# Optimization experiments

Hardware: AMD Instinct MI355X
Metric: run time of the kernel (lower is better)

The kernel has to match this reference:

```python
import jax, jax.numpy as jnp
import numpy as np

N = 50000      # nodes
E = 800000     # edges (before self-loops)
F_IN = 128     # args.nsegment
H = 4          # args.nhead
C = 32         # args.dhidden
OUT = 64       # output_dim
G = 64         # number of graphs in batch
NEG = 0.2      # args.negslope (and GATv2 internal leaky-relu slope, PyG default 0.2)


def setup_inputs() -> dict:
    key = jax.random.key(0)
    ks = jax.random.split(key, 8)
    def w(k, i, o):
        return jax.random.normal(k, (i, o), jnp.float32) / np.sqrt(i)
    x = jax.random.normal(ks[0], (N, F_IN), jnp.float32)
    edge_index = jax.random.randint(ks[1], (2, E), 0, N, dtype=jnp.int32)
    batch = jnp.sort(jax.random.randint(ks[2], (N,), 0, G, dtype=jnp.int32))
    d = dict(x=x, edge_index=edge_index, batch=batch)
    # layer dims: (in_dim, heads, out_per_head, concat)
    dims = [(F_IN, H, C, True), (H * C, H, C, True), (H * C, 1, OUT, False)]
    for li, (fi, h, c, concat) in enumerate(dims):
        k1, k2, k3 = jax.random.split(ks[3 + li], 3)
        d[f"Wl{li}"] = w(k1, fi, h * c)
        d[f"Wr{li}"] = w(k2, fi, h * c)
        d[f"att{li}"] = jax.random.normal(k3, (h, c), jnp.float32) / np.sqrt(c)
        d[f"b{li}"] = jnp.zeros((h * c if concat else c,), jnp.float32)
    return d


def _gat_layer(x, src, tgt, Wl, Wr, att, b, concat):
    """GATv2Conv: e_ij = att . leaky_relu(Wl x_j + Wr x_i); softmax over edges into i;
    out_i = sum_j alpha_ij * (Wl x_j). src/tgt include self-loops."""
    n = x.shape[0]
    h, c = att.shape
    xl = (x @ Wl).reshape(n, h, c)                 # source transform [N,h,c]
    xr = (x @ Wr).reshape(n, h, c)                 # target transform [N,h,c]
    g = jax.nn.leaky_relu(xl[src] + xr[tgt], NEG)  # [Etot,h,c]
    score = jnp.einsum('ehc,hc->eh', g, att)       # [Etot,h]
    smax = jax.ops.segment_max(score, tgt, num_segments=n)
    ex = jnp.exp(score - smax[tgt])
    den = jax.ops.segment_sum(ex, tgt, num_segments=n)
    alpha = ex / den[tgt]                          # per-target softmax [Etot,h]
    out = jax.ops.segment_sum(xl[src] * alpha[:, :, None], tgt, num_segments=n)
    out = out.reshape(n, h * c) if concat else out.mean(axis=1)
    return out + b


def _forward(x, edge_index, batch, params):
    n = x.shape[0]
    loops = jnp.arange(n, dtype=edge_index.dtype)  # PyG add_self_loops=True
    src = jnp.concatenate([edge_index[0], loops])
    tgt = jnp.concatenate([edge_index[1], loops])
    for Wl, Wr, att, b, concat in params:
        x = _gat_layer(x, src, tgt, Wl, Wr, att, b, concat)
        x = jax.nn.leaky_relu(x, NEG)  # dropout p is identity in eval mode
    ssum = jax.ops.segment_sum(x, batch, num_segments=G)
    cnt = jax.ops.segment_sum(jnp.ones((n,), x.dtype), batch, num_segments=G)
    return ssum / jnp.maximum(cnt, 1.0)[:, None]   # global_mean_pool -> [G, OUT]


def reference(x, edge_index, batch, Wl0, Wr0, att0, b0, Wl1, Wr1, att1, b1, Wl2, Wr2, att2, b2):
    params = [(Wl0, Wr0, att0, b0, True),
              (Wl1, Wr1, att1, b1, True),
              (Wl2, Wr2, att2, b2, False)]
    return _forward(x, edge_index, batch, params)
```

## Files before the change

kernel.cpp:

```cpp
#include <hip/hip_runtime.h>
#include <hip/hip_fp16.h>
#include <math.h>

#define NEGSLOPE 0.2f

__device__ __forceinline__ float lrelu(float x) { return x > 0.f ? x : NEGSLOPE * x; }

__global__ void k_count(const int* __restrict__ tgt, int* __restrict__ deg, int e) {
    int i = blockIdx.x * 256 + threadIdx.x;
    if (i < e) atomicAdd(&deg[tgt[i]], 1);
}
__global__ __launch_bounds__(256) void k_scanA(const int* __restrict__ deg, int* __restrict__ rowptr,
                                               int* __restrict__ bsums, int n) {
    __shared__ int s[256];
    int t = threadIdx.x;
    int base = blockIdx.x * 4096 + t * 16;
    int pre[16];
    int sum = 0;
    for (int i = 0; i < 16; ++i) {
        int idx = base + i;
        int v = (idx < n) ? (deg[idx] + 1) : 0;
        pre[i] = sum;
        sum += v;
    }
    s[t] = sum;
    __syncthreads();
    for (int off = 1; off < 256; off <<= 1) {
        int v = (t >= off) ? s[t - off] : 0;
        __syncthreads();
        s[t] += v;
        __syncthreads();
    }
    int tbase = s[t] - sum;
    for (int i = 0; i < 16; ++i) {
        int idx = base + i;
        if (idx < n) rowptr[idx] = tbase + pre[i];
    }
    if (t == 0) bsums[blockIdx.x] = s[255];
}
__global__ void k_scanB(int* __restrict__ bsums, int* __restrict__ rowptr, int nblk, int n) {
    if (threadIdx.x == 0 && blockIdx.x == 0) {
        int run = 0;
        for (int i = 0; i < nblk; ++i) { int v = bsums[i]; bsums[i] = run; run += v; }
        rowptr[n] = run;
    }
}
__global__ void k_scanC(int* __restrict__ rowptr, const int* __restrict__ bsums,
                        int* __restrict__ edst, int* __restrict__ cursor, int n) {
    int i = blockIdx.x * 256 + threadIdx.x;
    if (i < n) {
        int rp = rowptr[i] + bsums[i >> 12];
        rowptr[i] = rp;
        edst[rp] = i;
        cursor[i] = rp + 1;
    }
}
__global__ void k_scatter(const int* __restrict__ src, const int* __restrict__ tgt,
                          int* __restrict__ cursor, int* __restrict__ edst, int e) {
    int i = blockIdx.x * 256 + threadIdx.x;
    if (i < e) { int p = atomicAdd(&cursor[tgt[i]], 1); edst[p] = src[i]; }
}

template<int KOUT>
__global__ __launch_bounds__(256) void k_gemm_fused(const float* __restrict__ Ain,
        const float* __restrict__ W0, const float* __restrict__ W1,
        __half* __restrict__ out0, float* __restrict__ out1, int n) {
    __shared__ float Ast[32][132];
    __shared__ float Wt[32][132];
    int t = threadIdx.x;
    int ct = blockIdx.y;
    int w = t >> 6, lane = t & 63;
    int rg = (lane >> 3) + 8 * (w & 1);
    int cg = (lane & 7) + 8 * (w >> 1);
    int r0 = rg * 8, c0 = cg * 8;
    int row0 = blockIdx.x * 128;

    float acc[8][8] = {};
    for (int kc = 0; kc < 4; ++kc) {
        int kb = kc * 32;
        __syncthreads();
        for (int i = 0; i < 4; ++i) {
            int idx = t + 256 * i;
            int r = idx >> 3, kq = idx & 7;
            float4 v = make_float4(0.f, 0.f, 0.f, 0.f);
            int gr = row0 + r;
            if (gr < n) v = *(const float4*)(Ain + (size_t)gr * 128 + kb + 4 * kq);
            Ast[4 * kq + 0][r] = v.x; Ast[4 * kq + 1][r] = v.y;
            Ast[4 * kq + 2][r] = v.z; Ast[4 * kq + 3][r] = v.w;
        }
        for (int i = 0; i < 4; ++i) {
            int idx = t + 256 * i;
            int k = idx >> 5, cq = idx & 31;
            float4 v;
            if (KOUT == 128) {
                const float* W = ct ? W1 : W0;
                v = *(const float4*)(W + (size_t)(kb + k) * 128 + 4 * cq);
            } else {
                const float* W = (cq < 16) ? W0 : W1;
                int c = (cq < 16) ? 4 * cq : 4 * (cq - 16);
                v = *(const float4*)(W + (size_t)(kb + k) * 64 + c);
            }
            *(float4*)&Wt[k][4 * cq] = v;
        }
        __syncthreads();
#pragma unroll 2
        for (int k = 0; k < 32; ++k) {
            float a_[8], b_[8];
            *(float4*)&a_[0] = *(const float4*)&Ast[k][r0];
            *(float4*)&a_[4] = *(const float4*)&Ast[k][r0 + 4];
            *(float4*)&b_[0] = *(const float4*)&Wt[k][c0];
            *(float4*)&b_[4] = *(const float4*)&Wt[k][c0 + 4];
#pragma unroll
            for (int i = 0; i < 8; ++i)
#pragma unroll
                for (int j = 0; j < 8; ++j)
                    acc[i][j] += a_[i] * b_[j];
        }
    }
    bool asHalf = (KOUT == 128) ? (ct == 0) : (cg < 8);
    int c = (KOUT == 128) ? c0 : ((cg < 8) ? c0 : c0 - 64);
    for (int i = 0; i < 8; ++i) {
        int gr = row0 + r0 + i;
        if (gr >= n) break;
        if (asHalf) {
            union { uint4 u; __half2 h[4]; } pk;
#pragma unroll
            for (int j = 0; j < 4; ++j)
                pk.h[j] = __float22half2_rn(make_float2(acc[i][2 * j], acc[i][2 * j + 1]));
            *(uint4*)(out0 + (size_t)gr * KOUT + c) = pk.u;
        } else {
            *(float4*)(out1 + (size_t)gr * KOUT + c)     = *(float4*)&acc[i][0];
            *(float4*)(out1 + (size_t)gr * KOUT + c + 4) = *(float4*)&acc[i][4];
        }
    }
}

template<int H, int C>
__global__ __launch_bounds__(256) void k_agg(const __half* __restrict__ xl, const float* __restrict__ xr,
                                             const float* __restrict__ att, const float* __restrict__ bias,
                                             const int* __restrict__ rowptr, const int* __restrict__ edst,
                                             float* __restrict__ yout, int n) {
    constexpr int F = H * C;
    constexpr int VEC = F / 16;
    constexpr int L = C / VEC;
    int lane = threadIdx.x & 63;
    int wave = threadIdx.x >> 6;
    int s = lane & 15;
    int node = blockIdx.x * 16 + wave * 4 + (lane >> 4);
    bool valid = node < n;
    int nodeSafe = valid ? node : 0;
    int ch = s * VEC;

    float u[VEC], av[VEC], acc[VEC];
#pragma unroll
    for (int j = 0; j < VEC; ++j) {
        u[j] = xr[(size_t)nodeSafe * F + ch + j];
        av[j] = att[ch + j];
        acc[j] = 0.f;
    }
    int e0 = rowptr[nodeSafe];
    int deg = valid ? (rowptr[nodeSafe + 1] - e0) : 0;
    int maxdeg = deg;
    maxdeg = max(maxdeg, __shfl_xor(maxdeg, 16));
    maxdeg = max(maxdeg, __shfl_xor(maxdeg, 32));
    float ssum = 0.f;

    auto loadrow = [&](int src, float* v) {
        const __half* p = xl + (size_t)src * F + ch;
        if constexpr (VEC == 8) {
            union { uint4 u4; __half2 h[4]; } pk;
            pk.u4 = *(const uint4*)p;
#pragma unroll
            for (int j = 0; j < 4; ++j) {
                float2 f = __half22float2(pk.h[j]);
                v[2 * j] = f.x; v[2 * j + 1] = f.y;
            }
        } else {
            union { uint2 u2; __half2 h[2]; } pk;
            pk.u2 = *(const uint2*)p;
#pragma unroll
            for (int j = 0; j < 2; ++j) {
                float2 f = __half22float2(pk.h[j]);
                v[2 * j] = f.x; v[2 * j + 1] = f.y;
            }
        }
    };
    auto dot = [&](const float* v) {
        float p = 0.f;
#pragma unroll
        for (int j = 0; j < VEC; ++j) p += lrelu(v[j] + u[j]) * av[j];
        return p;
    };
    auto accum = [&](float w, const float* v) {
        ssum += w;
#pragma unroll
        for (int j = 0; j < VEC; ++j) acc[j] += w * v[j];
    };

    for (int base = 0; base < maxdeg; base += 16) {
        int cnt = deg - base;
        if (cnt > 16) cnt = 16;
        int idxreg = (s < cnt) ? edst[e0 + base + s] : nodeSafe;
        int mcnt = cnt;
        mcnt = max(mcnt, __shfl_xor(mcnt, 16));
        mcnt = max(mcnt, __shfl_xor(mcnt, 32));
        int gbase = lane & 48;
        int i = 0;
        for (; i + 4 <= mcnt; i += 4) {
            int s0 = __shfl(idxreg, gbase + i);
            int s1 = __shfl(idxreg, gbase + i + 1);
            int s2 = __shfl(idxreg, gbase + i + 2);
            int s3 = __shfl(idxreg, gbase + i + 3);
            float v0[VEC], v1[VEC], v2[VEC], v3[VEC];
            loadrow(s0, v0); loadrow(s1, v1); loadrow(s2, v2); loadrow(s3, v3);
            float p0 = dot(v0), p1 = dot(v1), p2 = dot(v2), p3 = dot(v3);
#pragma unroll
            for (int off = 1; off < L; off <<= 1) {
                p0 += __shfl_xor(p0, off);
                p1 += __shfl_xor(p1, off);
                p2 += __shfl_xor(p2, off);
                p3 += __shfl_xor(p3, off);
            }
            float w0 = (i + 0 < cnt) ? __expf(p0) : 0.f;
            float w1 = (i + 1 < cnt) ? __expf(p1) : 0.f;
            float w2 = (i + 2 < cnt) ? __expf(p2) : 0.f;
            float w3 = (i + 3 < cnt) ? __expf(p3) : 0.f;
            accum(w0, v0); accum(w1, v1); accum(w2, v2); accum(w3, v3);
        }
        for (; i < mcnt; ++i) {
            int s0 = __shfl(idxreg, gbase + i);
            float v[VEC];
            loadrow(s0, v);
            float p = dot(v);
#pragma unroll
            for (int off = 1; off < L; off <<= 1) p += __shfl_xor(p, off);
            float w = (i < cnt) ? __expf(p) : 0.f;
            accum(w, v);
        }
    }
    if (valid) {
        float inv = 1.f / ssum;
        float o[VEC];
#pragma unroll
        for (int j = 0; j < VEC; ++j) o[j] = lrelu(acc[j] * inv + bias[ch + j]);
        float* p = yout + (size_t)node * F + ch;
        *(float4*)p = *(float4*)o;
        if constexpr (VEC == 8) *(float4*)(p + 4) = *(float4*)(o + 4);
    }
}

__global__ __launch_bounds__(256) void k_pool_partial(const float* __restrict__ y,
        const int* __restrict__ batch, float* __restrict__ pacc, int n, int nchunk) {
    __shared__ float sdata[256];
    __shared__ int range[2];
    int g = blockIdx.x;
    int chunk = blockIdx.y;
    int t = threadIdx.x;
    if (t == 0) {
        int lo = 0, hi = n;
        while (lo < hi) { int mid = (lo + hi) >> 1; if (batch[mid] < g) lo = mid + 1; else hi = mid; }
        range[0] = lo;
        hi = n;
        while (lo < hi) { int mid = (lo + hi) >> 1; if (batch[mid] < g + 1) lo = mid + 1; else hi = mid; }
        range[1] = lo;
    }
    __syncthreads();
    int start = range[0], len = range[1] - range[0];
    int lo = start + (int)((long long)len * chunk / nchunk);
    int hi = start + (int)((long long)len * (chunk + 1) / nchunk);
    int ch = t & 63, sub = t >> 6;
    float acc = 0.f;
    for (int node = lo + sub; node < hi; node += 4)
        acc += y[(size_t)node * 64 + ch];
    sdata[t] = acc;
    __syncthreads();
    if (t < 128) sdata[t] += sdata[t + 128];
    __syncthreads();
    if (t < 64) atomicAdd(&pacc[g * 64 + t], sdata[t] + sdata[t + 64]);
}
__global__ void k_pool_final(const float* __restrict__ pacc, const int* __restrict__ batch,
                             float* __restrict__ out, int n) {
    __shared__ int cntS;
    int g = blockIdx.x, t = threadIdx.x;
    if (t == 0) {
        int lo = 0, hi = n;
        while (lo < hi) { int mid = (lo + hi) >> 1; if (batch[mid] < g) lo = mid + 1; else hi = mid; }
        int s = lo;
        hi = n;
        while (lo < hi) { int mid = (lo + hi) >> 1; if (batch[mid] < g + 1) lo = mid + 1; else hi = mid; }
        cntS = lo - s;
    }
    __syncthreads();
    out[g * 64 + t] = pacc[g * 64 + t] / fmaxf((float)cntS, 1.f);
}

extern "C" void kernel_launch(void* const* d_in, const int* in_sizes, int n_in,
                              void* d_out, int out_size, void* d_ws, size_t ws_size,
                              hipStream_t stream) {
    const float* x     = (const float*)d_in[0];
    const int*   ei    = (const int*)d_in[1];
    const int*   batch = (const int*)d_in[2];
    const float* Wl0 = (const float*)d_in[3];
    const float* Wr0 = (const float*)d_in[4];
    const float* att0 = (const float*)d_in[5];
    const float* b0  = (const float*)d_in[6];
    const float* Wl1 = (const float*)d_in[7];
    const float* Wr1 = (const float*)d_in[8];
    const float* att1 = (const float*)d_in[9];
    const float* b1  = (const float*)d_in[10];
    const float* Wl2 = (const float*)d_in[11];
    const float* Wr2 = (const float*)d_in[12];
    const float* att2 = (const float*)d_in[13];
    const float* b2  = (const float*)d_in[14];

    const int N = in_sizes[2];
    const int E = in_sizes[1] / 2;
    const int G = out_size / 64;
    const int* src = ei;
    const int* tgt = ei + E;

    size_t off = 0;
    auto take = [&](size_t bytes) {
        void* p = (char*)d_ws + off;
        off = (off + bytes + 255) & ~(size_t)255;
        return p;
    };
    __half* A   = (__half*)take((size_t)N * 128 * 2);
    float* B    = (float*)take((size_t)N * 128 * 4);
    float* Cb   = (float*)take((size_t)N * 128 * 4);
    int* rowptr = (int*)take((size_t)(N + 1) * 4);
    int* tmp    = (int*)take((size_t)N * 4);
    float* pacc = (float*)take((size_t)G * 64 * 4);
    int* edst   = (int*)take((size_t)(E + N) * 4);
    int* bsums  = (int*)take(64 * 4);
    (void)ws_size; (void)n_in;

    const int TB = 256;
    int nblkN = (N + TB - 1) / TB;
    int nblkE = (E + TB - 1) / TB;
    int nscan = (N + 4095) / 4096;

    hipMemsetAsync(tmp, 0, (size_t)((char*)(pacc + G * 64) - (char*)tmp), stream);

    k_count<<<nblkE, TB, 0, stream>>>(tgt, tmp, E);
    k_scanA<<<nscan, TB, 0, stream>>>(tmp, rowptr, bsums, N);
    k_scanB<<<1, 64, 0, stream>>>(bsums, rowptr, nscan, N);
    k_scanC<<<nblkN, TB, 0, stream>>>(rowptr, bsums, edst, tmp, N);
    k_scatter<<<nblkE, TB, 0, stream>>>(src, tgt, tmp, edst, E);

    int gemmBlocks = (N + 127) / 128;
    dim3 gemmGrid2(gemmBlocks, 2);
    dim3 gemmGrid1(gemmBlocks, 1);
    int aggBlocks = (N + 15) / 16;

    k_gemm_fused<128><<<gemmGrid2, TB, 0, stream>>>(x, Wl0, Wr0, A, B, N);
    k_agg<4, 32><<<aggBlocks, TB, 0, stream>>>(A, B, att0, b0, rowptr, edst, Cb, N);

    k_gemm_fused<128><<<gemmGrid2, TB, 0, stream>>>(Cb, Wl1, Wr1, A, B, N);
    k_agg<4, 32><<<aggBlocks, TB, 0, stream>>>(A, B, att1, b1, rowptr, edst, Cb, N);

    k_gemm_fused<64><<<gemmGrid1, TB, 0, stream>>>(Cb, Wl2, Wr2, A, B, N);
    k_agg<1, 64><<<aggBlocks, TB, 0, stream>>>(A, B, att2, b2, rowptr, edst, Cb, N);

    dim3 poolGrid(G, 16);
    k_pool_partial<<<poolGrid, TB, 0, stream>>>(Cb, batch, pacc, N, 16);
    k_pool_final<<<G, 64, 0, stream>>>(pacc, batch, (float*)d_out, N);
}
```

Measured before the change: 442.4 us.

## Replace FP32 SIMT GEMMs with FP16 MFMA and store intermediate activations in half

The shared-memory FP32 register-tiled GEMM is replaced by a kernel that uses the 16x16x32 f16 MFMA instruction. It reads FP16 activations and pre-transposed FP16 weights straight from global memory. New conversion kernels cast the input features and all six weight matrices to FP16. The aggregation kernel now writes FP16 outputs for the first two layers, which halves the intermediate traffic. The cost is two extra conversion launches, FP16 precision loss on inputs and weights, and scalar strided output stores from the MFMA kernel.

```diff
diff --git a/kernel.cpp b/kernel.cpp
--- a/kernel.cpp
+++ b/kernel.cpp
@@ -3,6 +3,9 @@
 #include <math.h>
 
 #define NEGSLOPE 0.2f
+
+typedef _Float16 f16x8 __attribute__((ext_vector_type(8)));
+typedef float f32x4 __attribute__((ext_vector_type(4)));
 
 __device__ __forceinline__ float lrelu(float x) { return x > 0.f ? x : NEGSLOPE * x; }
 
@@ -61,85 +64,81 @@
     if (i < e) { int p = atomicAdd(&cursor[tgt[i]], 1); edst[p] = src[i]; }
 }
 
+__global__ void k_xconv(const float* __restrict__ x, _Float16* __restrict__ xh, int n8) {
+    int i = blockIdx.x * 256 + threadIdx.x;
+    if (i < n8) {
+        float4 a = ((const float4*)x)[2 * i], b = ((const float4*)x)[2 * i + 1];
+        union { uint4 u; _Float16 h[8]; } pk;
+        pk.h[0] = (_Float16)a.x; pk.h[1] = (_Float16)a.y;
+        pk.h[2] = (_Float16)a.z; pk.h[3] = (_Float16)a.w;
+        pk.h[4] = (_Float16)b.x; pk.h[5] = (_Float16)b.y;
+        pk.h[6] = (_Float16)b.z; pk.h[7] = (_Float16)b.w;
+        ((uint4*)xh)[i] = pk.u;
+    }
+}
+__global__ void k_wconv(const float* W0, const float* W1, const float* W2,
+                        const float* W3, const float* W4, const float* W5,
+                        _Float16* D0, _Float16* D1, _Float16* D2,
+                        _Float16* D3, _Float16* D4, _Float16* D5) {
+    int b = blockIdx.x, k = threadIdx.x;
+    const float* src; _Float16* dst; int col, kout;
+    if (b < 128)      { src = W0; dst = D0; col = b;       kout = 128; }
+    else if (b < 256) { src = W1; dst = D1; col = b - 128; kout = 128; }
+    else if (b < 384) { src = W2; dst = D2; col = b - 256; kout = 128; }
+    else if (b < 512) { src = W3; dst = D3; col = b - 384; kout = 128; }
+    else if (b < 576) { src = W4; dst = D4; col = b - 512; kout = 64; }
+    else              { src = W5; dst = D5; col = b - 576; kout = 64; }
+    dst[col * 128 + k] = (_Float16)src[k * kout + col];
+}
+
 template<int KOUT>
-__global__ __launch_bounds__(256) void k_gemm_fused(const float* __restrict__ Ain,
-        const float* __restrict__ W0, const float* __restrict__ W1,
-        __half* __restrict__ out0, float* __restrict__ out1, int n) {
-    __shared__ float Ast[32][132];
-    __shared__ float Wt[32][132];
-    int t = threadIdx.x;
-    int ct = blockIdx.y;
-    int w = t >> 6, lane = t & 63;
-    int rg = (lane >> 3) + 8 * (w & 1);
-    int cg = (lane & 7) + 8 * (w >> 1);
-    int r0 = rg * 8, c0 = cg * 8;
-    int row0 = blockIdx.x * 128;
-
-    float acc[8][8] = {};
-    for (int kc = 0; kc < 4; ++kc) {
-        int kb = kc * 32;
-        __syncthreads();
+__global__ __launch_bounds__(256) void k_gemm_mfma(
+        const _Float16* __restrict__ Ah,
+        const _Float16* __restrict__ Wt0, const _Float16* __restrict__ Wt1,
+        _Float16* __restrict__ out0, float* __restrict__ out1, int n) {
+    int wv = threadIdx.x >> 6, lane = threadIdx.x & 63;
+    int m = lane & 15, q = lane >> 4;
+    int row0 = blockIdx.x * 64 + wv * 16;
+    int arow = row0 + m; if (arow >= n) arow = n - 1;
+    const _Float16* ap = Ah + (size_t)arow * 128 + q * 8;
+    f16x8 af[4];
+#pragma unroll
+    for (int kt = 0; kt < 4; ++kt) af[kt] = *(const f16x8*)(ap + 32 * kt);
+
+    f32x4 acc[8] = {};
+    const _Float16* Wsel = Wt0;
+    if (KOUT == 128 && blockIdx.y) Wsel = Wt1;
+#pragma unroll
+    for (int kt = 0; kt < 4; ++kt) {
+#pragma unroll
+        for (int ct = 0; ct < 8; ++ct) {
+            const _Float16* W = (KOUT == 128) ? Wsel : (ct < 4 ? Wt0 : Wt1);
+            int col0 = (KOUT == 128) ? ct * 16 : (ct & 3) * 16;
+            f16x8 bf = *(const f16x8*)(W + (size_t)(col0 + m) * 128 + 32 * kt + 8 * q);
+            acc[ct] = __builtin_amdgcn_mfma_f32_16x16x32_f16(af[kt], bf, acc[ct], 0, 0, 0);
+        }
+    }
+#pragma unroll
+    for (int ct = 0; ct < 8; ++ct) {
+        bool asHalf = (KOUT == 128) ? (blockIdx.y == 0) : (ct < 4);
+        int col0 = (KOUT == 128) ? ct * 16 : (ct & 3) * 16;
+        int col = col0 + m;
+#pragma unroll
         for (int i = 0; i < 4; ++i) {
-            int idx = t + 256 * i;
-            int r = idx >> 3, kq = idx & 7;
-            float4 v = make_float4(0.f, 0.f, 0.f, 0.f);
-            int gr = row0 + r;
-            if (gr < n) v = *(const float4*)(Ain + (size_t)gr * 128 + kb + 4 * kq);
-            Ast[4 * kq + 0][r] = v.x; Ast[4 * kq + 1][r] = v.y;
-            Ast[4 * kq + 2][r] = v.z; Ast[4 * kq + 3][r] = v.w;
-        }
-        for (int i = 0; i < 4; ++i) {
-            int idx = t + 256 * i;
-            int k = idx >> 5, cq = idx & 31;
-            float4 v;
-            if (KOUT == 128) {
-                const float* W = ct ? W1 : W0;
-                v = *(const float4*)(W + (size_t)(kb + k) * 128 + 4 * cq);
-            } else {
-                const float* W = (cq < 16) ? W0 : W1;
-                int c = (cq < 16) ? 4 * cq : 4 * (cq - 16);
-                v = *(const float4*)(W + (size_t)(kb + k) * 64 + c);
-            }
-            *(float4*)&Wt[k][4 * cq] = v;
-        }
-        __syncthreads();
-#pragma unroll 2
-        for (int k = 0; k < 32; ++k) {
-            float a_[8], b_[8];
-            *(float4*)&a_[0] = *(const float4*)&Ast[k][r0];
-            *(float4*)&a_[4] = *(const float4*)&Ast[k][r0 + 4];
-            *(float4*)&b_[0] = *(const float4*)&Wt[k][c0];
-            *(float4*)&b_[4] = *(const float4*)&Wt[k][c0 + 4];
-#pragma unroll
-            for (int i = 0; i < 8; ++i)
-#pragma unroll
-                for (int j = 0; j < 8; ++j)
-                    acc[i][j] += a_[i] * b_[j];
-        }
-    }
-    bool asHalf = (KOUT == 128) ? (ct == 0) : (cg < 8);
-    int c = (KOUT == 128) ? c0 : ((cg < 8) ? c0 : c0 - 64);
-    for (int i = 0; i < 8; ++i) {
-        int gr = row0 + r0 + i;
-        if (gr >= n) break;
-        if (asHalf) {
-            union { uint4 u; __half2 h[4]; } pk;
-#pragma unroll
-            for (int j = 0; j < 4; ++j)
-                pk.h[j] = __float22half2_rn(make_float2(acc[i][2 * j], acc[i][2 * j + 1]));
-            *(uint4*)(out0 + (size_t)gr * KOUT + c) = pk.u;
-        } else {
-            *(float4*)(out1 + (size_t)gr * KOUT + c)     = *(float4*)&acc[i][0];
-            *(float4*)(out1 + (size_t)gr * KOUT + c + 4) = *(float4*)&acc[i][4];
-        }
-    }
-}
-
-template<int H, int C>
+            int r = row0 + q * 4 + i;
+            if (r < n) {
+                if (asHalf) out0[(size_t)r * KOUT + col] = (_Float16)acc[ct][i];
+                else        out1[(size_t)r * KOUT + col] = acc[ct][i];
+            }
+        }
+    }
+}
+
+template<int H, int C, typename OutT>
 __global__ __launch_bounds__(256) void k_agg(const __half* __restrict__ xl, const float* __restrict__ xr,
                                              const float* __restrict__ att, const float* __restrict__ bias,
                                              const int* __restrict__ rowptr, const int* __restrict__ edst,
-                                             float* __restrict__ yout, int n) {
+                                             OutT* __restrict__ yout, int n) {
     constexpr int F = H * C;
     constexpr int VEC = F / 16;
     constexpr int L = C / VEC;
@@ -243,9 +242,25 @@
         float o[VEC];
 #pragma unroll
         for (int j = 0; j < VEC; ++j) o[j] = lrelu(acc[j] * inv + bias[ch + j]);
-        float* p = yout + (size_t)node * F + ch;
-        *(float4*)p = *(float4*)o;
-        if constexpr (VEC == 8) *(float4*)(p + 4) = *(float4*)(o + 4);
+        if constexpr (sizeof(OutT) == 2) {
+            _Float16* p = (_Float16*)yout + (size_t)node * F + ch;
+            if constexpr (VEC == 8) {
+                union { uint4 u; _Float16 h[8]; } pk;
+#pragma unroll
+                for (int j = 0; j < 8; ++j) pk.h[j] = (_Float16)o[j];
+                *(uint4*)p = pk.u;
+            } else {
+                union { uint2 u; _Float16 h[4]; } pk;
+#pragma unroll
+                for (int j = 0; j < 4; ++j) pk.h[j] = (_Float16)o[j];
+                *(uint2*)p = pk.u;
+            }
+        } else {
+            float* p = (float*)yout + (size_t)node * F + ch;
+            *(float4*)p = make_float4(o[0], o[1], o[2], o[3]);
+            if constexpr (VEC == 8)
+                *(float4*)(p + 4) = make_float4(o[4], o[5], o[6], o[7]);
+        }
     }
 }
 
@@ -325,9 +340,17 @@
         off = (off + bytes + 255) & ~(size_t)255;
         return p;
     };
-    __half* A   = (__half*)take((size_t)N * 128 * 2);
-    float* B    = (float*)take((size_t)N * 128 * 4);
-    float* Cb   = (float*)take((size_t)N * 128 * 4);
+    _Float16* xh   = (_Float16*)take((size_t)N * 128 * 2);
+    _Float16* Ah   = (_Float16*)take((size_t)N * 128 * 2);
+    float* B       = (float*)take((size_t)N * 128 * 4);
+    _Float16* Cbh  = (_Float16*)take((size_t)N * 128 * 2);
+    float* Cbf     = (float*)take((size_t)N * 64 * 4);
+    _Float16* Wl0t = (_Float16*)take(128 * 128 * 2);
+    _Float16* Wr0t = (_Float16*)take(128 * 128 * 2);
+    _Float16* Wl1t = (_Float16*)take(128 * 128 * 2);
+    _Float16* Wr1t = (_Float16*)take(128 * 128 * 2);
+    _Float16* Wl2t = (_Float16*)take(64 * 128 * 2);
+    _Float16* Wr2t = (_Float16*)take(64 * 128 * 2);
     int* rowptr = (int*)take((size_t)(N + 1) * 4);
     int* tmp    = (int*)take((size_t)N * 4);
     float* pacc = (float*)take((size_t)G * 64 * 4);
@@ -348,21 +371,25 @@
     k_scanC<<<nblkN, TB, 0, stream>>>(rowptr, bsums, edst, tmp, N);
     k_scatter<<<nblkE, TB, 0, stream>>>(src, tgt, tmp, edst, E);
 
-    int gemmBlocks = (N + 127) / 128;
+    k_xconv<<<(N * 128 / 8 + TB - 1) / TB, TB, 0, stream>>>(x, xh, N * 128 / 8);
+    k_wconv<<<640, 128, 0, stream>>>(Wl0, Wr0, Wl1, Wr1, Wl2, Wr2,
+                                     Wl0t, Wr0t, Wl1t, Wr1t, Wl2t, Wr2t);
+
+    int gemmBlocks = (N + 63) / 64;
     dim3 gemmGrid2(gemmBlocks, 2);
     dim3 gemmGrid1(gemmBlocks, 1);
     int aggBlocks = (N + 15) / 16;
 
-    k_gemm_fused<128><<<gemmGrid2, TB, 0, stream>>>(x, Wl0, Wr0, A, B, N);
-    k_agg<4, 32><<<aggBlocks, TB, 0, stream>>>(A, B, att0, b0, rowptr, edst, Cb, N);
-
-    k_gemm_fused<128><<<gemmGrid2, TB, 0, stream>>>(Cb, Wl1, Wr1, A, B, N);
-    k_agg<4, 32><<<aggBlocks, TB, 0, stream>>>(A, B, att1, b1, rowptr, edst, Cb, N);
-
-    k_gemm_fused<64><<<gemmGrid1, TB, 0, stream>>>(Cb, Wl2, Wr2, A, B, N);
-    k_agg<1, 64><<<aggBlocks, TB, 0, stream>>>(A, B, att2, b2, rowptr, edst, Cb, N);
+    k_gemm_mfma<128><<<gemmGrid2, TB, 0, stream>>>(xh, Wl0t, Wr0t, Ah, B, N);
+    k_agg<4, 32, _Float16><<<aggBlocks, TB, 0, stream>>>((const __half*)Ah, B, att0, b0, rowptr, edst, Cbh, N);
+
+    k_gemm_mfma<128><<<gemmGrid2, TB, 0, stream>>>(Cbh, Wl1t, Wr1t, Ah, B, N);
+    k_agg<4, 32, _Float16><<<aggBlocks, TB, 0, stream>>>((const __half*)Ah, B, att1, b1, rowptr, edst, Cbh, N);
+
+    k_gemm_mfma<64><<<gemmGrid1, TB, 0, stream>>>(Cbh, Wl2t, Wr2t, Ah, B, N);
+    k_agg<1, 64, float><<<aggBlocks, TB, 0, stream>>>((const __half*)Ah, B, att2, b2, rowptr, edst, Cbf, N);
 
     dim3 poolGrid(G, 16);
-    k_pool_partial<<<poolGrid, TB, 0, stream>>>(Cb, batch, pacc, N, 16);
+    k_pool_partial<<<poolGrid, TB, 0, stream>>>(Cbf, batch, pacc, N, 16);
     k_pool_final<<<G, 64, 0, stream>>>(pacc, batch, (float*)d_out, N);
 }
```

After: 412.9 us. 1.07x faster.
